# Kernel tuning notes

Measured on AMD Instinct MI355X. Metric: run time of the kernel, lower is better.

## Reference

```python
import jax, jax.numpy as jnp
import numpy as np

POINT_DIM, VOXEL_DIM, NUM_HEADS = 3, 256, 8
HEAD_DIM = VOXEL_DIM // NUM_HEADS


def _linear_params(key, fan_in, fan_out):
    kw, kb = jax.random.split(key)
    bound = 1.0 / np.sqrt(fan_in)
    W = jax.random.uniform(kw, (fan_out, fan_in), jnp.float32, -bound, bound)
    b = jax.random.uniform(kb, (fan_out,), jnp.float32, -bound, bound)
    return W, b


def setup_inputs() -> dict:
    key = jax.random.key(0)
    ks = jax.random.split(key, 7)
    points = jax.random.normal(ks[0], (2, 4096, POINT_DIM), jnp.float32)
    voxel_features = jax.random.normal(ks[1], (2, 2048, VOXEL_DIM), jnp.float32)
    Wp, bp = _linear_params(ks[2], POINT_DIM, VOXEL_DIM)
    Wq, bq = _linear_params(ks[3], VOXEL_DIM, VOXEL_DIM)
    Wk, bk = _linear_params(ks[4], VOXEL_DIM, VOXEL_DIM)
    Wv, bv = _linear_params(ks[5], VOXEL_DIM, VOXEL_DIM)
    Wf, bf = _linear_params(ks[6], VOXEL_DIM * 2, VOXEL_DIM)
    return {
        "points": points, "voxel_features": voxel_features,
        "Wp": Wp, "bp": bp, "Wq": Wq, "bq": bq,
        "Wk": Wk, "bk": bk, "Wv": Wv, "bv": bv,
        "Wf": Wf, "bf": bf,
    }


def reference(points, voxel_features, Wp, bp, Wq, bq, Wk, bk, Wv, bv, Wf, bf):
    B, N, _ = points.shape
    M = voxel_features.shape[1]
    # projections (torch Linear: x @ W.T + b)
    point_features = points @ Wp.T + bp                      # [B,N,D]
    q = (point_features @ Wq.T + bq).reshape(B, N, NUM_HEADS, HEAD_DIM)
    k = (voxel_features @ Wk.T + bk).reshape(B, M, NUM_HEADS, HEAD_DIM)
    v = (voxel_features @ Wv.T + bv).reshape(B, M, NUM_HEADS, HEAD_DIM)
    # attention scores [B,H,N,M]
    scale = 1.0 / np.sqrt(HEAD_DIM).astype(np.float32)
    attn = jnp.einsum('bnhd,bmhd->bhnm', q, k) * scale
    attn = jax.nn.softmax(attn, axis=-1)
    attended = jnp.einsum('bhnm,bmhd->bnhd', attn, v).reshape(B, N, VOXEL_DIM)
    fused = jnp.concatenate([point_features, attended], axis=-1) @ Wf.T + bf
    return fused
```

## Files before the change

kernel.cpp:

```cpp
#include <hip/hip_runtime.h>

#define B_ 2
#define N_ 4096
#define M_ 2048
#define D_ 256
#define H_ 8
#define DH_ 32
#define ROWS_ (B_*N_)
#define KVROWS_ (B_*M_)
#define PRE_ (0.17677669529663687f * 1.4426950408889634f)
#define CBASE_ 32.0f

typedef __attribute__((ext_vector_type(8))) short short8_t;
typedef __attribute__((ext_vector_type(4))) float float4_t;

#if defined(__has_builtin)
# if __has_builtin(__builtin_amdgcn_exp2f)
#  define EXP2F(x) __builtin_amdgcn_exp2f(x)
# else
#  define EXP2F(x) exp2f(x)
# endif
#else
# define EXP2F(x) exp2f(x)
#endif

__device__ __forceinline__ unsigned int rne_u(float f) {
    union { float f; unsigned int u; } c;
    c.f = f;
    return c.u + 0x7FFFu + ((c.u >> 16) & 1u);
}

__device__ __forceinline__ unsigned short f2us(float f) {
    return (unsigned short)(rne_u(f) >> 16);
}

__device__ __forceinline__ unsigned int pack2rn(float a, float b) {
    return __builtin_amdgcn_perm(rne_u(b), rne_u(a), 0x07060302u);
}

__device__ __forceinline__ unsigned int pack2tr(float a, float b) {
    union { float f; unsigned int u; } x, y;
    x.f = a; y.f = b;
    return __builtin_amdgcn_perm(y.u, x.u, 0x07060302u);
}

__device__ __forceinline__ short8_t cvt8(float4 a, float4 b) {
    union { unsigned int u[4]; short8_t s; } c;
    c.u[0] = pack2rn(a.x, a.y);
    c.u[1] = pack2rn(a.z, a.w);
    c.u[2] = pack2rn(b.x, b.y);
    c.u[3] = pack2rn(b.z, b.w);
    return c.s;
}

__device__ __forceinline__ int xcd_swz(int bid, int nwg) {
    const int cpx = nwg >> 3;
    return (bid & 7) * cpx + (bid >> 3);
}

template<int K, int NCOL, int LDSRC>
__device__ __forceinline__ void stageB2(const float* __restrict__ W, int col0, int kof,
                                        unsigned short* __restrict__ Bs, int tid)
{
    const int n = tid & (NCOL - 1), g = tid / NCOL;
    const int GROUPS = 256 / NCOL;
    const int CPT = (K / 8) / GROUPS;
    const float* src = W + (size_t)(col0 + n) * LDSRC + kof + g * (K / GROUPS);
#pragma unroll
    for (int ci = 0; ci < CPT; ci++) {
        int logc = g * CPT + ci;
        int phys = logc ^ (n & 7);
        short8_t v = cvt8(*(const float4*)(src + ci * 8), *(const float4*)(src + ci * 8 + 4));
        *(short8_t*)(Bs + (size_t)n * K + phys * 8) = v;
    }
}

template<int K>
__device__ __forceinline__ short8_t readB(const unsigned short* __restrict__ Bs,
                                          int c, int l16, int quad, int k0)
{
    int phys = ((k0 >> 3) + quad) ^ (l16 & 7);
    return *(const short8_t*)(Bs + (size_t)(16 * c + l16) * K + phys * 8);
}

__global__ __launch_bounds__(256) void g_projkv4(
    const float* __restrict__ voxel,
    const float* __restrict__ Wp, const float* __restrict__ bp,
    const float* __restrict__ Wq, const float* __restrict__ bq,
    const float* __restrict__ Wk, const float* __restrict__ bk,
    const float* __restrict__ Wv, const float* __restrict__ bv,
    const float* __restrict__ Wf, const float* __restrict__ bfb,
    unsigned short* __restrict__ k_g, unsigned short* __restrict__ vt_g,
    float* __restrict__ Wqc, float* __restrict__ Wfc)
{
    const int tid = threadIdx.x;
    const int wave = tid >> 6, lane = tid & 63, quad = lane >> 4, l16 = lane & 15;

    __shared__ unsigned short Bs[64 * 256];

    const int bid = (int)blockIdx.x;
    if (bid < 512) {
        const int lbid = xcd_swz(bid, 512);
        const int row0 = (lbid >> 3) * 64;
        const int sub  = lbid & 7;
        const int col0 = (sub >> 1) * 64;
        const bool isV = sub & 1;

        stageB2<256, 64, 256>(isV ? Wv : Wk, col0, 0, Bs, tid);

        const float* arow = voxel + (size_t)(row0 + wave * 16 + l16) * D_;
        short8_t af[8];
#pragma unroll
        for (int i = 0; i < 8; i++)
            af[i] = cvt8(*(const float4*)(arow + i * 32 + quad * 8),
                         *(const float4*)(arow + i * 32 + quad * 8 + 4));

        float4_t acc[4];
#pragma unroll
        for (int c = 0; c < 4; c++) acc[c] = (float4_t){0.f, 0.f, 0.f, 0.f};
        __syncthreads();
#pragma unroll
        for (int i = 0; i < 8; i++)
#pragma unroll
            for (int c = 0; c < 4; c++)
                acc[c] = __builtin_amdgcn_mfma_f32_16x16x32_bf16(af[i], readB<256>(Bs, c, l16, quad, i * 32), acc[c], 0, 0, 0);

        if (!isV) {
#pragma unroll
            for (int c = 0; c < 4; c++) {
                int col = col0 + 16 * c + l16;
                float bbk = bk[col];
#pragma unroll
                for (int r = 0; r < 4; r++) {
                    int row = row0 + wave * 16 + quad * 4 + r;
                    k_g[(size_t)row * D_ + col] = f2us(acc[c][r] + bbk);
                }
            }
        } else {
            const int b = row0 / M_;
            const int m0 = row0 - b * M_ + wave * 16 + quad * 4;
#pragma unroll
            for (int c = 0; c < 4; c++) {
                int col = col0 + 16 * c + l16;
                float bbv = bv[col];
                int h = col >> 5, dh = col & 31;
                unsigned int u0 = pack2rn(acc[c][0] + bbv, acc[c][1] + bbv);
                unsigned int u1 = pack2rn(acc[c][2] + bbv, acc[c][3] + bbv);
                *(uint2*)(vt_g + (size_t)((b * H_ + h) * DH_ + dh) * M_ + m0) = make_uint2(u0, u1);
            }
        }
    } else {
        const int role = bid - 512;
        float* wps = (float*)Bs;
        *(float4*)(wps + tid * 4) = make_float4(Wp[tid * 3 + 0], Wp[tid * 3 + 1],
                                                Wp[tid * 3 + 2], bp[tid]);
        __syncthreads();
        const int col = tid;
        const float* wrow = role ? (Wf + (size_t)col * 512) : (Wq + (size_t)col * 256);
        float a0 = 0.f, a1 = 0.f, a2 = 0.f, ab = 0.f;
#pragma unroll 4
        for (int d = 0; d < 256; d += 4) {
            float4 wv = *(const float4*)(wrow + d);
            float4 w0 = *(const float4*)(wps + (d + 0) * 4);
            float4 w1 = *(const float4*)(wps + (d + 1) * 4);
            float4 w2 = *(const float4*)(wps + (d + 2) * 4);
            float4 w3 = *(const float4*)(wps + (d + 3) * 4);
            a0 += wv.x * w0.x + wv.y * w1.x + wv.z * w2.x + wv.w * w3.x;
            a1 += wv.x * w0.y + wv.y * w1.y + wv.z * w2.y + wv.w * w3.y;
            a2 += wv.x * w0.z + wv.y * w1.z + wv.z * w2.z + wv.w * w3.z;
            ab += wv.x * w0.w + wv.y * w1.w + wv.z * w2.w + wv.w * w3.w;
        }
        if (role == 0) {
            *(float4*)(Wqc + (size_t)col * 4) =
                make_float4(a0 * PRE_, a1 * PRE_, a2 * PRE_, (ab + bq[col]) * PRE_);
        } else {
            *(float4*)(Wfc + (size_t)col * 4) =
                make_float4(a0, a1, a2, ab + bfb[col]);
        }
    }
}

__global__ __launch_bounds__(512) void k_attn11(
    const float* __restrict__ points, const float* __restrict__ Wqc,
    const unsigned short* __restrict__ k_g,
    const unsigned short* __restrict__ vt_g,
    unsigned short* __restrict__ att_g)
{
    const int tid = threadIdx.x;
    const int w = tid >> 6, lane = tid & 63, quad = lane >> 4, l16 = lane & 15;
    const int lbid = xcd_swz((int)blockIdx.x, B_ * H_ * (N_ / 128));
    const int nt = lbid & 31;
    const int bh = lbid >> 5;
    const int b = bh >> 3, h = bh & 7;
    const int n0 = nt * 128 + w * 16;

    __shared__ unsigned short Kt[4][64][40];
    __shared__ unsigned short Vt[4][32][72];

    const unsigned short* kbase = k_g + (size_t)(b * M_) * D_ + h * DH_;
    const unsigned short* vbase = vt_g + (size_t)(bh * DH_) * M_;

    const bool isK = (tid < 256);
    const int kr = tid >> 2, kc = tid & 3;
    const int vr = (tid - 256) >> 3, vc = tid & 7;
    const int ksr = kr ^ ((kr & 8) >> 1);

    const int gstep = isK ? 64 * D_ : 64;
    const unsigned short* gq = isK ? (kbase + (size_t)kr * D_ + kc * 8)
                                   : (vbase + (size_t)vr * M_ + vc * 8);
    unsigned short* ldst = isK ? (&Kt[0][0][0] + ksr * 40 + kc * 8)
                               : (&Vt[0][0][0] + vr * 72 + vc * 8);
    const int lstride = isK ? 2560 : 2304;

    *(short8_t*)ldst = *(const short8_t*)gq;
    gq += gstep;
    *(short8_t*)(ldst + lstride) = *(const short8_t*)gq;

    const int rbas = 8 * (l16 >> 2) + (l16 & 3);
    const int rx = l16 & 4;
    int krow[4];
#pragma unroll
    for (int t = 0; t < 4; t++)
        krow[t] = (rbas + 4 * (t & 1) + 32 * (t >> 1)) ^ rx;

    const size_t qrow = (size_t)(b * N_ + n0 + l16);
    const float p0 = points[qrow * 3 + 0];
    const float p1 = points[qrow * 3 + 1];
    const float p2 = points[qrow * 3 + 2];
    float q8[8];
#pragma unroll
    for (int j = 0; j < 8; j++) {
        float4 wc = *(const float4*)(Wqc + (size_t)(h * DH_ + quad * 8 + j) * 4);
        q8[j] = p0 * wc.x + p1 * wc.y + p2 * wc.z + wc.w;
    }
    short8_t qf = cvt8(make_float4(q8[0], q8[1], q8[2], q8[3]),
                       make_float4(q8[4], q8[5], q8[6], q8[7]));

    short8_t ones;
#pragma unroll
    for (int j = 0; j < 8; j++) ones[j] = (short)0x3F80;

    float4_t od0 = {0.f, 0.f, 0.f, 0.f};
    float4_t od1 = {0.f, 0.f, 0.f, 0.f};
    float4_t lacc = {0.f, 0.f, 0.f, 0.f};

    const float4_t zc = {-CBASE_, -CBASE_, -CBASE_, -CBASE_};

    __syncthreads();

#define STEPC(KB_, VB_)                                                         \
    do {                                                                        \
        float4_t st[4];                                                         \
        _Pragma("unroll")                                                       \
        for (int t = 0; t < 4; t++) {                                           \
            short8_t kf = *(const short8_t*)&Kt[KB_][krow[t]][quad * 8];        \
            st[t] = __builtin_amdgcn_mfma_f32_16x16x32_bf16(kf, qf, zc, 0, 0, 0); \
        }                                                                       \
        unsigned int uu[4][2];                                                  \
        _Pragma("unroll")                                                       \
        for (int t = 0; t < 4; t++) {                                           \
            float e0 = EXP2F(st[t][0]);                                         \
            float e1 = EXP2F(st[t][1]);                                         \
            float e2 = EXP2F(st[t][2]);                                         \
            float e3 = EXP2F(st[t][3]);                                         \
            uu[t][0] = pack2tr(e0, e1);                                         \
            uu[t][1] = pack2tr(e2, e3);                                         \
        }                                                                       \
        union { unsigned int u[4]; short8_t s; } pa, pb2;                       \
        pa.u[0]  = uu[0][0]; pa.u[1]  = uu[0][1];                               \
        pa.u[2]  = uu[1][0]; pa.u[3]  = uu[1][1];                               \
        pb2.u[0] = uu[2][0]; pb2.u[1] = uu[2][1];                               \
        pb2.u[2] = uu[3][0]; pb2.u[3] = uu[3][1];                               \
        lacc = __builtin_amdgcn_mfma_f32_16x16x32_bf16(ones, pa.s,  lacc, 0, 0, 0); \
        lacc = __builtin_amdgcn_mfma_f32_16x16x32_bf16(ones, pb2.s, lacc, 0, 0, 0); \
        short8_t vf00 = *(const short8_t*)&Vt[VB_][l16][quad * 8];              \
        short8_t vf01 = *(const short8_t*)&Vt[VB_][l16][32 + quad * 8];         \
        short8_t vf10 = *(const short8_t*)&Vt[VB_][16 + l16][quad * 8];         \
        short8_t vf11 = *(const short8_t*)&Vt[VB_][16 + l16][32 + quad * 8];    \
        od0 = __builtin_amdgcn_mfma_f32_16x16x32_bf16(vf00, pa.s,  od0, 0, 0, 0); \
        od0 = __builtin_amdgcn_mfma_f32_16x16x32_bf16(vf01, pb2.s, od0, 0, 0, 0); \
        od1 = __builtin_amdgcn_mfma_f32_16x16x32_bf16(vf10, pa.s,  od1, 0, 0, 0); \
        od1 = __builtin_amdgcn_mfma_f32_16x16x32_bf16(vf11, pb2.s, od1, 0, 0, 0); \
    } while (0)

#pragma unroll 2
    for (int s = 0; s < M_ / 64; s += 2) {
        const bool m0 = (s + 2 < M_ / 64);
        const bool m1 = (s + 3 < M_ / 64);
        short8_t nxt0, nxt1;
        if (m0) { gq += gstep; nxt0 = *(const short8_t*)gq; }
        if (m1) { gq += gstep; nxt1 = *(const short8_t*)gq; }

        STEPC((s) & 3, (s) & 3);
        STEPC((s + 1) & 3, (s + 1) & 3);

        if (m0) *(short8_t*)(ldst + ((s + 2) & 3) * lstride) = nxt0;
        if (m1) *(short8_t*)(ldst + ((s + 3) & 3) * lstride) = nxt1;
        __syncthreads();
    }
#undef STEPC

    const float inv = 1.0f / lacc[0];

    unsigned short* ob = att_g + (size_t)(b * N_ + n0 + l16) * D_ + h * DH_;
    {
        unsigned int u0 = pack2rn(od0[0] * inv, od0[1] * inv);
        unsigned int u1 = pack2rn(od0[2] * inv, od0[3] * inv);
        *(uint2*)(ob + quad * 4) = make_uint2(u0, u1);
        unsigned int u2 = pack2rn(od1[0] * inv, od1[1] * inv);
        unsigned int u3 = pack2rn(od1[2] * inv, od1[3] * inv);
        *(uint2*)(ob + 16 + quad * 4) = make_uint2(u2, u3);
    }
}

__global__ __launch_bounds__(256) void g_fuse3(
    const unsigned short* __restrict__ att_g,
    const float* __restrict__ points, const float* __restrict__ Wfc,
    const float* __restrict__ Wf,
    float* __restrict__ out)
{
    const int tid = threadIdx.x;
    const int wave = tid >> 6, lane = tid & 63, quad = lane >> 4, l16 = lane & 15;
    const int lbid = xcd_swz((int)blockIdx.x, (ROWS_ / 64) * 4);
    const int row0 = (lbid >> 2) * 64;
    const int col0 = (lbid & 3) * 64;

    __shared__ unsigned short Bs[64 * 256];

    stageB2<256, 64, 512>(Wf, col0, 256, Bs, tid);
    __syncthreads();

    float4_t acc[4];
#pragma unroll
    for (int c = 0; c < 4; c++) acc[c] = (float4_t){0.f, 0.f, 0.f, 0.f};

    const size_t arow = (size_t)(row0 + wave * 16 + l16) * D_;
#pragma unroll
    for (int k0 = 0; k0 < 256; k0 += 32) {
        short8_t af = *(const short8_t*)(att_g + arow + k0 + quad * 8);
#pragma unroll
        for (int c = 0; c < 4; c++)
            acc[c] = __builtin_amdgcn_mfma_f32_16x16x32_bf16(af, readB<256>(Bs, c, l16, quad, k0), acc[c], 0, 0, 0);
    }

    const int rbase = row0 + wave * 16 + quad * 4;
    float px[4], py[4], pz[4];
#pragma unroll
    for (int r = 0; r < 4; r++) {
        px[r] = points[(size_t)(rbase + r) * 3 + 0];
        py[r] = points[(size_t)(rbase + r) * 3 + 1];
        pz[r] = points[(size_t)(rbase + r) * 3 + 2];
    }
#pragma unroll
    for (int c = 0; c < 4; c++) {
        int col = col0 + 16 * c + l16;
        float4 wf = *(const float4*)(Wfc + (size_t)col * 4);
#pragma unroll
        for (int r = 0; r < 4; r++) {
            out[(size_t)(rbase + r) * D_ + col] =
                acc[c][r] + px[r] * wf.x + py[r] * wf.y + pz[r] * wf.z + wf.w;
        }
    }
}

extern "C" void kernel_launch(void* const* d_in, const int* in_sizes, int n_in,
                              void* d_out, int out_size, void* d_ws, size_t ws_size,
                              hipStream_t stream)
{
    const float* points = (const float*)d_in[0];
    const float* voxel  = (const float*)d_in[1];
    const float* Wp  = (const float*)d_in[2];
    const float* bp  = (const float*)d_in[3];
    const float* Wq  = (const float*)d_in[4];
    const float* bq  = (const float*)d_in[5];
    const float* Wk  = (const float*)d_in[6];
    const float* bk  = (const float*)d_in[7];
    const float* Wv  = (const float*)d_in[8];
    const float* bv  = (const float*)d_in[9];
    const float* Wf  = (const float*)d_in[10];
    const float* bfb = (const float*)d_in[11];
    float* out = (float*)d_out;

    float* Wqc = (float*)d_ws;
    float* Wfc = Wqc + 256 * 4;
    unsigned short* k_g   = (unsigned short*)(Wfc + 256 * 4);
    unsigned short* vt_g  = k_g  + (size_t)KVROWS_ * D_;
    unsigned short* att_g = vt_g + (size_t)KVROWS_ * D_;

    g_projkv4<<<dim3(514), dim3(256), 0, stream>>>(voxel, Wp, bp, Wq, bq, Wk, bk,
                                                   Wv, bv, Wf, bfb, k_g, vt_g, Wqc, Wfc);
    k_attn11<<<dim3(B_ * H_ * (N_ / 128)), dim3(512), 0, stream>>>(points, Wqc, k_g, vt_g, att_g);
    g_fuse3 <<<dim3((ROWS_ / 64) * 4), dim3(256), 0, stream>>>(att_g, points, Wfc, Wf, out);
}
```

Before: 132.1 us.

## Fold query projection into keys to cut attention score dot to rank four

Since each query is an affine function of three point coordinates, q·k equals [p,1]·(Wqc^T k). The projection kernel now computes a per-head four-element vector per key, Wqc^T k, instead of storing full K rows. The attention kernel then loads this compact kq tile for the whole sequence into LDS once and computes scores with a masked MFMA. This removes the K stream and its double-buffered staging from the attention loop and leaves only V streaming, so LDS per block shrinks and launch bounds are raised for occupancy. In exchange, the projection epilogue gains a shuffle reduction and a serial Wqc prologue. Scores are also computed from bf16-rounded products, which may change numerical accuracy.

```diff
diff --git a/kernel.cpp b/kernel.cpp
--- a/kernel.cpp
+++ b/kernel.cpp
@@ -83,20 +83,21 @@
     return *(const short8_t*)(Bs + (size_t)(16 * c + l16) * K + phys * 8);
 }
 
-__global__ __launch_bounds__(256) void g_projkv4(
+__global__ __launch_bounds__(256) void g_projkv5(
     const float* __restrict__ voxel,
     const float* __restrict__ Wp, const float* __restrict__ bp,
     const float* __restrict__ Wq, const float* __restrict__ bq,
     const float* __restrict__ Wk, const float* __restrict__ bk,
     const float* __restrict__ Wv, const float* __restrict__ bv,
     const float* __restrict__ Wf, const float* __restrict__ bfb,
-    unsigned short* __restrict__ k_g, unsigned short* __restrict__ vt_g,
-    float* __restrict__ Wqc, float* __restrict__ Wfc)
+    unsigned short* __restrict__ kq_g, unsigned short* __restrict__ vt_g,
+    float* __restrict__ Wfc)
 {
     const int tid = threadIdx.x;
     const int wave = tid >> 6, lane = tid & 63, quad = lane >> 4, l16 = lane & 15;
 
     __shared__ unsigned short Bs[64 * 256];
+    __shared__ float Wqc_l[64 * 4];
 
     const int bid = (int)blockIdx.x;
     if (bid < 512) {
@@ -106,6 +107,42 @@
         const int col0 = (sub >> 1) * 64;
         const bool isV = sub & 1;
 
+        if (!isV) {
+            float* wps = (float*)Bs;
+            float* P4  = (float*)Bs + 1024;
+            *(float4*)(wps + tid * 4) = make_float4(Wp[tid * 3 + 0], Wp[tid * 3 + 1],
+                                                    Wp[tid * 3 + 2], bp[tid]);
+            __syncthreads();
+            {
+                const int cc = tid >> 2, part = tid & 3;
+                const float* wrow = Wq + (size_t)(col0 + cc) * 256 + part * 64;
+                const float* wpp = wps + part * 256;
+                float a0 = 0.f, a1 = 0.f, a2 = 0.f, ab = 0.f;
+#pragma unroll 4
+                for (int e = 0; e < 64; e++) {
+                    float wv = wrow[e];
+                    float4 aa = *(const float4*)(wpp + e * 4);
+                    a0 += wv * aa.x; a1 += wv * aa.y; a2 += wv * aa.z; ab += wv * aa.w;
+                }
+                *(float4*)(P4 + (size_t)tid * 4) = make_float4(a0, a1, a2, ab);
+            }
+            __syncthreads();
+            if (tid < 64) {
+                float4 s0 = *(const float4*)(P4 + (tid * 4 + 0) * 4);
+                float4 s1 = *(const float4*)(P4 + (tid * 4 + 1) * 4);
+                float4 s2 = *(const float4*)(P4 + (tid * 4 + 2) * 4);
+                float4 s3 = *(const float4*)(P4 + (tid * 4 + 3) * 4);
+                float a0 = (s0.x + s1.x) + (s2.x + s3.x);
+                float a1 = (s0.y + s1.y) + (s2.y + s3.y);
+                float a2 = (s0.z + s1.z) + (s2.z + s3.z);
+                float ab = (s0.w + s1.w) + (s2.w + s3.w);
+                *(float4*)(Wqc_l + tid * 4) =
+                    make_float4(a0 * PRE_, a1 * PRE_, a2 * PRE_,
+                                (ab + bq[col0 + tid]) * PRE_);
+            }
+            __syncthreads();
+        }
+
         stageB2<256, 64, 256>(isV ? Wv : Wk, col0, 0, Bs, tid);
 
         const float* arow = voxel + (size_t)(row0 + wave * 16 + l16) * D_;
@@ -125,18 +162,7 @@
             for (int c = 0; c < 4; c++)
                 acc[c] = __builtin_amdgcn_mfma_f32_16x16x32_bf16(af[i], readB<256>(Bs, c, l16, quad, i * 32), acc[c], 0, 0, 0);
 
-        if (!isV) {
-#pragma unroll
-            for (int c = 0; c < 4; c++) {
-                int col = col0 + 16 * c + l16;
-                float bbk = bk[col];
-#pragma unroll
-                for (int r = 0; r < 4; r++) {
-                    int row = row0 + wave * 16 + quad * 4 + r;
-                    k_g[(size_t)row * D_ + col] = f2us(acc[c][r] + bbk);
-                }
-            }
-        } else {
+        if (isV) {
             const int b = row0 / M_;
             const int m0 = row0 - b * M_ + wave * 16 + quad * 4;
 #pragma unroll
@@ -148,15 +174,60 @@
                 unsigned int u1 = pack2rn(acc[c][2] + bbv, acc[c][3] + bbv);
                 *(uint2*)(vt_g + (size_t)((b * H_ + h) * DH_ + dh) * M_ + m0) = make_uint2(u0, u1);
             }
+        } else {
+            float bkv[4];
+#pragma unroll
+            for (int c = 0; c < 4; c++) bkv[c] = bk[col0 + 16 * c + l16];
+            float4 wq0 = *(const float4*)(Wqc_l + l16 * 4);
+            float4 wq1 = *(const float4*)(Wqc_l + (16 + l16) * 4);
+            float4 wq2 = *(const float4*)(Wqc_l + (32 + l16) * 4);
+            float4 wq3 = *(const float4*)(Wqc_l + (48 + l16) * 4);
+            const float* q0 = (const float*)&wq0;
+            const float* q1 = (const float*)&wq1;
+            const float* q2 = (const float*)&wq2;
+            const float* q3 = (const float*)&wq3;
+            float pA[4][4], pB[4][4];
+#pragma unroll
+            for (int r = 0; r < 4; r++) {
+                float kA0 = acc[0][r] + bkv[0], kA1 = acc[1][r] + bkv[1];
+                float kB0 = acc[2][r] + bkv[2], kB1 = acc[3][r] + bkv[3];
+#pragma unroll
+                for (int j = 0; j < 4; j++) {
+                    pA[r][j] = kA0 * q0[j] + kA1 * q1[j];
+                    pB[r][j] = kB0 * q2[j] + kB1 * q3[j];
+                }
+            }
+#pragma unroll
+            for (int m = 1; m < 16; m <<= 1)
+#pragma unroll
+                for (int r = 0; r < 4; r++)
+#pragma unroll
+                    for (int j = 0; j < 4; j++) {
+                        pA[r][j] += __shfl_xor(pA[r][j], m);
+                        pB[r][j] += __shfl_xor(pB[r][j], m);
+                    }
+            if (l16 == 0) {
+                const int b = row0 >> 11;
+                const int m0 = (row0 & (M_ - 1)) + wave * 16 + quad * 4;
+                const int hA = col0 >> 5;
+#pragma unroll
+                for (int r = 0; r < 4; r++) {
+                    unsigned int u0 = pack2rn(pA[r][0], pA[r][1]);
+                    unsigned int u1 = pack2rn(pA[r][2], pA[r][3]);
+                    *(uint2*)(kq_g + ((size_t)(b * H_ + hA) * M_ + m0 + r) * 4) = make_uint2(u0, u1);
+                    unsigned int u2 = pack2rn(pB[r][0], pB[r][1]);
+                    unsigned int u3 = pack2rn(pB[r][2], pB[r][3]);
+                    *(uint2*)(kq_g + ((size_t)(b * H_ + hA + 1) * M_ + m0 + r) * 4) = make_uint2(u2, u3);
+                }
+            }
         }
     } else {
-        const int role = bid - 512;
         float* wps = (float*)Bs;
         *(float4*)(wps + tid * 4) = make_float4(Wp[tid * 3 + 0], Wp[tid * 3 + 1],
                                                 Wp[tid * 3 + 2], bp[tid]);
         __syncthreads();
         const int col = tid;
-        const float* wrow = role ? (Wf + (size_t)col * 512) : (Wq + (size_t)col * 256);
+        const float* wrow = Wf + (size_t)col * 512;
         float a0 = 0.f, a1 = 0.f, a2 = 0.f, ab = 0.f;
 #pragma unroll 4
         for (int d = 0; d < 256; d += 4) {
@@ -170,91 +241,77 @@
             a2 += wv.x * w0.z + wv.y * w1.z + wv.z * w2.z + wv.w * w3.z;
             ab += wv.x * w0.w + wv.y * w1.w + wv.z * w2.w + wv.w * w3.w;
         }
-        if (role == 0) {
-            *(float4*)(Wqc + (size_t)col * 4) =
-                make_float4(a0 * PRE_, a1 * PRE_, a2 * PRE_, (ab + bq[col]) * PRE_);
-        } else {
-            *(float4*)(Wfc + (size_t)col * 4) =
-                make_float4(a0, a1, a2, ab + bfb[col]);
-        }
-    }
-}
-
-__global__ __launch_bounds__(512) void k_attn11(
-    const float* __restrict__ points, const float* __restrict__ Wqc,
-    const unsigned short* __restrict__ k_g,
+        *(float4*)(Wfc + (size_t)col * 4) = make_float4(a0, a1, a2, ab + bfb[col]);
+    }
+}
+
+__global__ __launch_bounds__(512, 8) void k_attn12(
+    const float* __restrict__ points,
+    const unsigned short* __restrict__ kq_g,
     const unsigned short* __restrict__ vt_g,
     unsigned short* __restrict__ att_g)
 {
     const int tid = threadIdx.x;
     const int w = tid >> 6, lane = tid & 63, quad = lane >> 4, l16 = lane & 15;
-    const int lbid = xcd_swz((int)blockIdx.x, B_ * H_ * (N_ / 128));
+    const int lbid = xcd_swz((int)blockIdx.x, 512);
     const int nt = lbid & 31;
     const int bh = lbid >> 5;
-    const int b = bh >> 3, h = bh & 7;
+    const int b = bh >> 3;
     const int n0 = nt * 128 + w * 16;
 
-    __shared__ unsigned short Kt[4][64][40];
-    __shared__ unsigned short Vt[4][32][72];
-
-    const unsigned short* kbase = k_g + (size_t)(b * M_) * D_ + h * DH_;
-    const unsigned short* vbase = vt_g + (size_t)(bh * DH_) * M_;
-
-    const bool isK = (tid < 256);
-    const int kr = tid >> 2, kc = tid & 3;
-    const int vr = (tid - 256) >> 3, vc = tid & 7;
-    const int ksr = kr ^ ((kr & 8) >> 1);
-
-    const int gstep = isK ? 64 * D_ : 64;
-    const unsigned short* gq = isK ? (kbase + (size_t)kr * D_ + kc * 8)
-                                   : (vbase + (size_t)vr * M_ + vc * 8);
-    unsigned short* ldst = isK ? (&Kt[0][0][0] + ksr * 40 + kc * 8)
-                               : (&Vt[0][0][0] + vr * 72 + vc * 8);
-    const int lstride = isK ? 2560 : 2304;
-
-    *(short8_t*)ldst = *(const short8_t*)gq;
-    gq += gstep;
-    *(short8_t*)(ldst + lstride) = *(const short8_t*)gq;
-
-    const int rbas = 8 * (l16 >> 2) + (l16 & 3);
-    const int rx = l16 & 4;
-    int krow[4];
-#pragma unroll
-    for (int t = 0; t < 4; t++)
-        krow[t] = (rbas + 4 * (t & 1) + 32 * (t >> 1)) ^ rx;
+    __shared__ unsigned short SL[17408];
+    unsigned short* kqL = SL;
+    unsigned short* Vt  = SL + 8192;
+
+    {
+        const unsigned short* ksrc = kq_g + (size_t)bh * (M_ * 4);
+        const int off = tid * 16;
+        *(short8_t*)(kqL + off)     = *(const short8_t*)(ksrc + off);
+        *(short8_t*)(kqL + off + 8) = *(const short8_t*)(ksrc + off + 8);
+    }
+
+    const unsigned short* vbase = vt_g + (size_t)bh * DH_ * M_;
+    const int vr = (tid & 255) >> 3, vc = tid & 7;
+    const int half = tid >> 8;
+    unsigned short* vdst = Vt + vr * 72 + vc * 8;
+    const unsigned short* gqv = vbase + (size_t)vr * M_ + vc * 8;
+    *(short8_t*)(vdst + half * 2304) = *(const short8_t*)(gqv + half * 64);
+    gqv += (2 + half) * 64;
 
     const size_t qrow = (size_t)(b * N_ + n0 + l16);
     const float p0 = points[qrow * 3 + 0];
     const float p1 = points[qrow * 3 + 1];
     const float p2 = points[qrow * 3 + 2];
-    float q8[8];
-#pragma unroll
-    for (int j = 0; j < 8; j++) {
-        float4 wc = *(const float4*)(Wqc + (size_t)(h * DH_ + quad * 8 + j) * 4);
-        q8[j] = p0 * wc.x + p1 * wc.y + p2 * wc.z + wc.w;
-    }
-    short8_t qf = cvt8(make_float4(q8[0], q8[1], q8[2], q8[3]),
-                       make_float4(q8[4], q8[5], q8[6], q8[7]));
+    const unsigned int um = (quad == 0) ? 0xFFFFFFFFu : 0u;
+    union { unsigned int u[4]; short8_t s; } qfu;
+    qfu.u[0] = pack2rn(p0, p1) & um;
+    qfu.u[1] = pack2rn(p2, 1.0f) & um;
+    qfu.u[2] = 0u; qfu.u[3] = 0u;
+    const short8_t qf = qfu.s;
 
     short8_t ones;
 #pragma unroll
     for (int j = 0; j < 8; j++) ones[j] = (short)0x3F80;
+
+    const unsigned short* kqp = kqL + (8 * (l16 >> 2) + (l16 & 3)) * 4;
 
     float4_t od0 = {0.f, 0.f, 0.f, 0.f};
     float4_t od1 = {0.f, 0.f, 0.f, 0.f};
     float4_t lacc = {0.f, 0.f, 0.f, 0.f};
-
     const float4_t zc = {-CBASE_, -CBASE_, -CBASE_, -CBASE_};
 
     __syncthreads();
 
-#define STEPC(KB_, VB_)                                                         \
+#define STEPC(VB_, KQP_)                                                        \
     do {                                                                        \
         float4_t st[4];                                                         \
         _Pragma("unroll")                                                       \
         for (int t = 0; t < 4; t++) {                                           \
-            short8_t kf = *(const short8_t*)&Kt[KB_][krow[t]][quad * 8];        \
-            st[t] = __builtin_amdgcn_mfma_f32_16x16x32_bf16(kf, qf, zc, 0, 0, 0); \
+            uint2 kv2 = *(const uint2*)((KQP_) + (t & 1) * 16 + (t >> 1) * 128);\
+            union { unsigned int u[4]; short8_t s; } afu;                       \
+            afu.u[0] = kv2.x & um; afu.u[1] = kv2.y & um;                       \
+            afu.u[2] = 0u; afu.u[3] = 0u;                                       \
+            st[t] = __builtin_amdgcn_mfma_f32_16x16x32_bf16(afu.s, qf, zc, 0, 0, 0); \
         }                                                                       \
         unsigned int uu[4][2];                                                  \
         _Pragma("unroll")                                                       \
@@ -267,16 +324,14 @@
             uu[t][1] = pack2tr(e2, e3);                                         \
         }                                                                       \
         union { unsigned int u[4]; short8_t s; } pa, pb2;                       \
-        pa.u[0]  = uu[0][0]; pa.u[1]  = uu[0][1];                               \
-        pa.u[2]  = uu[1][0]; pa.u[3]  = uu[1][1];                               \
-        pb2.u[0] = uu[2][0]; pb2.u[1] = uu[2][1];                               \
-        pb2.u[2] = uu[3][0]; pb2.u[3] = uu[3][1];                               \
+        pa.u[0]  = uu[0][0]; pa.u[1]  = uu[0][1]; pa.u[2]  = uu[1][0]; pa.u[3]  = uu[1][1]; \
+        pb2.u[0] = uu[2][0]; pb2.u[1] = uu[2][1]; pb2.u[2] = uu[3][0]; pb2.u[3] = uu[3][1]; \
         lacc = __builtin_amdgcn_mfma_f32_16x16x32_bf16(ones, pa.s,  lacc, 0, 0, 0); \
         lacc = __builtin_amdgcn_mfma_f32_16x16x32_bf16(ones, pb2.s, lacc, 0, 0, 0); \
-        short8_t vf00 = *(const short8_t*)&Vt[VB_][l16][quad * 8];              \
-        short8_t vf01 = *(const short8_t*)&Vt[VB_][l16][32 + quad * 8];         \
-        short8_t vf10 = *(const short8_t*)&Vt[VB_][16 + l16][quad * 8];         \
-        short8_t vf11 = *(const short8_t*)&Vt[VB_][16 + l16][32 + quad * 8];    \
+        short8_t vf00 = *(const short8_t*)(Vt + (VB_) * 2304 + l16 * 72 + quad * 8);        \
+        short8_t vf01 = *(const short8_t*)(Vt + (VB_) * 2304 + l16 * 72 + 32 + quad * 8);   \
+        short8_t vf10 = *(const short8_t*)(Vt + (VB_) * 2304 + (16 + l16) * 72 + quad * 8); \
+        short8_t vf11 = *(const short8_t*)(Vt + (VB_) * 2304 + (16 + l16) * 72 + 32 + quad * 8); \
         od0 = __builtin_amdgcn_mfma_f32_16x16x32_bf16(vf00, pa.s,  od0, 0, 0, 0); \
         od0 = __builtin_amdgcn_mfma_f32_16x16x32_bf16(vf01, pb2.s, od0, 0, 0, 0); \
         od1 = __builtin_amdgcn_mfma_f32_16x16x32_bf16(vf10, pa.s,  od1, 0, 0, 0); \
@@ -285,24 +340,25 @@
 
 #pragma unroll 2
     for (int s = 0; s < M_ / 64; s += 2) {
-        const bool m0 = (s + 2 < M_ / 64);
-        const bool m1 = (s + 3 < M_ / 64);
-        short8_t nxt0, nxt1;
-        if (m0) { gq += gstep; nxt0 = *(const short8_t*)gq; }
-        if (m1) { gq += gstep; nxt1 = *(const short8_t*)gq; }
-
-        STEPC((s) & 3, (s) & 3);
-        STEPC((s + 1) & 3, (s + 1) & 3);
-
-        if (m0) *(short8_t*)(ldst + ((s + 2) & 3) * lstride) = nxt0;
-        if (m1) *(short8_t*)(ldst + ((s + 3) & 3) * lstride) = nxt1;
+        const int tgt = s + 2 + half;
+        short8_t nxt;
+        if (tgt < M_ / 64) nxt = *(const short8_t*)gqv;
+
+        STEPC((s) & 3, kqp);
+        STEPC((s + 1) & 3, (kqp + 256));
+
+        if (tgt < M_ / 64) {
+            *(short8_t*)(vdst + (tgt & 3) * 2304) = nxt;
+            gqv += 128;
+        }
+        kqp += 512;
         __syncthreads();
     }
 #undef STEPC
 
     const float inv = 1.0f / lacc[0];
 
-    unsigned short* ob = att_g + (size_t)(b * N_ + n0 + l16) * D_ + h * DH_;
+    unsigned short* ob = att_g + (size_t)(b * N_ + n0 + l16) * D_ + (bh & 7) * DH_;
     {
         unsigned int u0 = pack2rn(od0[0] * inv, od0[1] * inv);
         unsigned int u1 = pack2rn(od0[2] * inv, od0[3] * inv);
@@ -381,14 +437,13 @@
     const float* bfb = (const float*)d_in[11];
     float* out = (float*)d_out;
 
-    float* Wqc = (float*)d_ws;
-    float* Wfc = Wqc + 256 * 4;
-    unsigned short* k_g   = (unsigned short*)(Wfc + 256 * 4);
-    unsigned short* vt_g  = k_g  + (size_t)KVROWS_ * D_;
+    float* Wfc = (float*)d_ws;
+    unsigned short* kq_g  = (unsigned short*)(Wfc + 256 * 4);
+    unsigned short* vt_g  = kq_g + (size_t)B_ * H_ * M_ * 4;
     unsigned short* att_g = vt_g + (size_t)KVROWS_ * D_;
 
-    g_projkv4<<<dim3(514), dim3(256), 0, stream>>>(voxel, Wp, bp, Wq, bq, Wk, bk,
-                                                   Wv, bv, Wf, bfb, k_g, vt_g, Wqc, Wfc);
-    k_attn11<<<dim3(B_ * H_ * (N_ / 128)), dim3(512), 0, stream>>>(points, Wqc, k_g, vt_g, att_g);
+    g_projkv5<<<dim3(513), dim3(256), 0, stream>>>(voxel, Wp, bp, Wq, bq, Wk, bk,
+                                                   Wv, bv, Wf, bfb, kq_g, vt_g, Wfc);
+    k_attn12<<<dim3(512), dim3(512), 0, stream>>>(points, kq_g, vt_g, att_g);
     g_fuse3 <<<dim3((ROWS_ / 64) * 4), dim3(256), 0, stream>>>(att_g, points, Wfc, Wf, out);
 }
```

After: 145.5 us. 1.1x slower.

## Split attention KV range in two and merge partial outputs in fuse kernel

Applied to the files above, without the earlier changes.

The attention kernel now splits the key/value sequence into two halves, doubling the grid so each block processes half of M. Each half writes unnormalized fp32 partial outputs and partial softmax denominators to workspace. The fusion kernel sums the two partials, normalizes, converts to bf16 and feeds the output GEMM. The aim is more parallelism and better CU fill, paid for with extra fp32 global memory traffic and a larger workspace; the merge is only correct because the softmax uses a fixed offset rather than a per-row running max.

```diff
diff --git a/kernel.cpp b/kernel.cpp
--- a/kernel.cpp
+++ b/kernel.cpp
@@ -8,6 +8,8 @@
 #define DH_ 32
 #define ROWS_ (B_*N_)
 #define KVROWS_ (B_*M_)
+#define ODHALF_ ((size_t)ROWS_*D_)
+#define LHALF_ ((size_t)B_*H_*N_)
 #define PRE_ (0.17677669529663687f * 1.4426950408889634f)
 #define CBASE_ 32.0f
 
@@ -180,25 +182,26 @@
     }
 }
 
-__global__ __launch_bounds__(512) void k_attn11(
+__global__ __launch_bounds__(512) void k_attn13(
     const float* __restrict__ points, const float* __restrict__ Wqc,
     const unsigned short* __restrict__ k_g,
     const unsigned short* __restrict__ vt_g,
-    unsigned short* __restrict__ att_g)
+    float* __restrict__ od_g, float* __restrict__ l_g)
 {
     const int tid = threadIdx.x;
     const int w = tid >> 6, lane = tid & 63, quad = lane >> 4, l16 = lane & 15;
-    const int lbid = xcd_swz((int)blockIdx.x, B_ * H_ * (N_ / 128));
-    const int nt = lbid & 31;
-    const int bh = lbid >> 5;
+    const int lbid = xcd_swz((int)blockIdx.x, B_ * H_ * (N_ / 128) * 2);
+    const int mh = lbid & 1;
+    const int nt = (lbid >> 1) & 31;
+    const int bh = lbid >> 6;
     const int b = bh >> 3, h = bh & 7;
     const int n0 = nt * 128 + w * 16;
 
     __shared__ unsigned short Kt[4][64][40];
     __shared__ unsigned short Vt[4][32][72];
 
-    const unsigned short* kbase = k_g + (size_t)(b * M_) * D_ + h * DH_;
-    const unsigned short* vbase = vt_g + (size_t)(bh * DH_) * M_;
+    const unsigned short* kbase = k_g + ((size_t)b * M_ + mh * (M_ / 2)) * D_ + h * DH_;
+    const unsigned short* vbase = vt_g + (size_t)bh * DH_ * M_ + mh * (M_ / 2);
 
     const bool isK = (tid < 256);
     const int kr = tid >> 2, kc = tid & 3;
@@ -284,9 +287,9 @@
     } while (0)
 
 #pragma unroll 2
-    for (int s = 0; s < M_ / 64; s += 2) {
-        const bool m0 = (s + 2 < M_ / 64);
-        const bool m1 = (s + 3 < M_ / 64);
+    for (int s = 0; s < M_ / 128; s += 2) {
+        const bool m0 = (s + 2 < M_ / 128);
+        const bool m1 = (s + 3 < M_ / 128);
         short8_t nxt0, nxt1;
         if (m0) { gq += gstep; nxt0 = *(const short8_t*)gq; }
         if (m1) { gq += gstep; nxt1 = *(const short8_t*)gq; }
@@ -300,21 +303,15 @@
     }
 #undef STEPC
 
-    const float inv = 1.0f / lacc[0];
-
-    unsigned short* ob = att_g + (size_t)(b * N_ + n0 + l16) * D_ + h * DH_;
-    {
-        unsigned int u0 = pack2rn(od0[0] * inv, od0[1] * inv);
-        unsigned int u1 = pack2rn(od0[2] * inv, od0[3] * inv);
-        *(uint2*)(ob + quad * 4) = make_uint2(u0, u1);
-        unsigned int u2 = pack2rn(od1[0] * inv, od1[1] * inv);
-        unsigned int u3 = pack2rn(od1[2] * inv, od1[3] * inv);
-        *(uint2*)(ob + 16 + quad * 4) = make_uint2(u2, u3);
-    }
-}
-
-__global__ __launch_bounds__(256) void g_fuse3(
-    const unsigned short* __restrict__ att_g,
+    float* obf = od_g + (size_t)mh * ODHALF_ + (size_t)(b * N_ + n0 + l16) * D_ + h * DH_;
+    *(float4_t*)(obf + quad * 4) = od0;
+    *(float4_t*)(obf + 16 + quad * 4) = od1;
+    if (quad == 0)
+        l_g[(size_t)mh * LHALF_ + (size_t)bh * N_ + n0 + l16] = lacc[0];
+}
+
+__global__ __launch_bounds__(256) void g_fuse4(
+    const float* __restrict__ od_g, const float* __restrict__ l_g,
     const float* __restrict__ points, const float* __restrict__ Wfc,
     const float* __restrict__ Wf,
     float* __restrict__ out)
@@ -328,16 +325,36 @@
     __shared__ unsigned short Bs[64 * 256];
 
     stageB2<256, 64, 512>(Wf, col0, 256, Bs, tid);
+
+    const int rowA = row0 + wave * 16 + l16;
+    const int bA = rowA >> 12, nA = rowA & (N_ - 1);
+    float inv[8];
+#pragma unroll
+    for (int hh = 0; hh < 8; hh++) {
+        size_t li = (size_t)(bA * H_ + hh) * N_ + nA;
+        inv[hh] = 1.0f / (l_g[li] + l_g[li + LHALF_]);
+    }
+
     __syncthreads();
 
     float4_t acc[4];
 #pragma unroll
     for (int c = 0; c < 4; c++) acc[c] = (float4_t){0.f, 0.f, 0.f, 0.f};
 
-    const size_t arow = (size_t)(row0 + wave * 16 + l16) * D_;
+    const size_t odrow = (size_t)rowA * D_;
 #pragma unroll
     for (int k0 = 0; k0 < 256; k0 += 32) {
-        short8_t af = *(const short8_t*)(att_g + arow + k0 + quad * 8);
+        const float iv = inv[k0 >> 5];
+        const float* pa = od_g + odrow + k0 + quad * 8;
+        float4 a0 = *(const float4*)(pa);
+        float4 a1 = *(const float4*)(pa + 4);
+        float4 c0 = *(const float4*)(pa + ODHALF_);
+        float4 c1 = *(const float4*)(pa + ODHALF_ + 4);
+        short8_t af = cvt8(
+            make_float4((a0.x + c0.x) * iv, (a0.y + c0.y) * iv,
+                        (a0.z + c0.z) * iv, (a0.w + c0.w) * iv),
+            make_float4((a1.x + c1.x) * iv, (a1.y + c1.y) * iv,
+                        (a1.z + c1.z) * iv, (a1.w + c1.w) * iv));
 #pragma unroll
         for (int c = 0; c < 4; c++)
             acc[c] = __builtin_amdgcn_mfma_f32_16x16x32_bf16(af, readB<256>(Bs, c, l16, quad, k0), acc[c], 0, 0, 0);
@@ -385,10 +402,11 @@
     float* Wfc = Wqc + 256 * 4;
     unsigned short* k_g   = (unsigned short*)(Wfc + 256 * 4);
     unsigned short* vt_g  = k_g  + (size_t)KVROWS_ * D_;
-    unsigned short* att_g = vt_g + (size_t)KVROWS_ * D_;
+    float* od_g = (float*)(vt_g + (size_t)KVROWS_ * D_);
+    float* l_g  = od_g + 2 * ODHALF_;
 
     g_projkv4<<<dim3(514), dim3(256), 0, stream>>>(voxel, Wp, bp, Wq, bq, Wk, bk,
                                                    Wv, bv, Wf, bfb, k_g, vt_g, Wqc, Wfc);
-    k_attn11<<<dim3(B_ * H_ * (N_ / 128)), dim3(512), 0, stream>>>(points, Wqc, k_g, vt_g, att_g);
-    g_fuse3 <<<dim3((ROWS_ / 64) * 4), dim3(256), 0, stream>>>(att_g, points, Wfc, Wf, out);
-}
+    k_attn13<<<dim3(B_ * H_ * (N_ / 128) * 2), dim3(512), 0, stream>>>(points, Wqc, k_g, vt_g, od_g, l_g);
+    g_fuse4 <<<dim3((ROWS_ / 64) * 4), dim3(256), 0, stream>>>(od_g, l_g, points, Wfc, Wf, out);
+}
```

After: 144.7 us. +9.5%, slower.

## Load K/V tiles directly from global into registers, dropping LDS staging

Applied to the files above, without the earlier changes.

The attention kernel no longer stages K and V tiles through shared memory with block-wide barriers. Each wave now loads its MFMA operand fragments straight from global memory into registers, using a two-deep register double buffer to overlap loads with compute. Block size is halved to 256 threads (64 query rows) with a doubled grid and a launch-bounds occupancy hint. This removes LDS traffic and __syncthreads, but each wave now fetches K/V independently, so global/L2 traffic rises about fourfold per query tile and the loads are less coalesced.

```diff
diff --git a/kernel.cpp b/kernel.cpp
--- a/kernel.cpp
+++ b/kernel.cpp
@@ -180,7 +180,7 @@
     }
 }
 
-__global__ __launch_bounds__(512) void k_attn11(
+__global__ __launch_bounds__(256, 4) void k_attn14(
     const float* __restrict__ points, const float* __restrict__ Wqc,
     const unsigned short* __restrict__ k_g,
     const unsigned short* __restrict__ vt_g,
@@ -188,40 +188,20 @@
 {
     const int tid = threadIdx.x;
     const int w = tid >> 6, lane = tid & 63, quad = lane >> 4, l16 = lane & 15;
-    const int lbid = xcd_swz((int)blockIdx.x, B_ * H_ * (N_ / 128));
-    const int nt = lbid & 31;
-    const int bh = lbid >> 5;
+    const int lbid = xcd_swz((int)blockIdx.x, B_ * H_ * (N_ / 64));
+    const int nt = lbid & 63;
+    const int bh = lbid >> 6;
     const int b = bh >> 3, h = bh & 7;
-    const int n0 = nt * 128 + w * 16;
-
-    __shared__ unsigned short Kt[4][64][40];
-    __shared__ unsigned short Vt[4][32][72];
+    const int n0 = nt * 64 + w * 16;
 
     const unsigned short* kbase = k_g + (size_t)(b * M_) * D_ + h * DH_;
-    const unsigned short* vbase = vt_g + (size_t)(bh * DH_) * M_;
-
-    const bool isK = (tid < 256);
-    const int kr = tid >> 2, kc = tid & 3;
-    const int vr = (tid - 256) >> 3, vc = tid & 7;
-    const int ksr = kr ^ ((kr & 8) >> 1);
-
-    const int gstep = isK ? 64 * D_ : 64;
-    const unsigned short* gq = isK ? (kbase + (size_t)kr * D_ + kc * 8)
-                                   : (vbase + (size_t)vr * M_ + vc * 8);
-    unsigned short* ldst = isK ? (&Kt[0][0][0] + ksr * 40 + kc * 8)
-                               : (&Vt[0][0][0] + vr * 72 + vc * 8);
-    const int lstride = isK ? 2560 : 2304;
-
-    *(short8_t*)ldst = *(const short8_t*)gq;
-    gq += gstep;
-    *(short8_t*)(ldst + lstride) = *(const short8_t*)gq;
-
-    const int rbas = 8 * (l16 >> 2) + (l16 & 3);
-    const int rx = l16 & 4;
-    int krow[4];
-#pragma unroll
-    for (int t = 0; t < 4; t++)
-        krow[t] = (rbas + 4 * (t & 1) + 32 * (t >> 1)) ^ rx;
+    const unsigned short* vbase = vt_g + (size_t)bh * DH_ * M_;
+
+    const int g0 = 8 * (l16 >> 2) + (l16 & 3);
+    const unsigned short* kp0 = kbase + (size_t)g0 * D_ + quad * 8;
+    const unsigned short* kp2 = kp0 + 32 * D_;
+    const unsigned short* vp0 = vbase + (size_t)l16 * M_ + quad * 8;
+    const unsigned short* vp1 = vp0 + (size_t)16 * M_;
 
     const size_t qrow = (size_t)(b * N_ + n0 + l16);
     const float p0 = points[qrow * 3 + 0];
@@ -243,19 +223,30 @@
     float4_t od0 = {0.f, 0.f, 0.f, 0.f};
     float4_t od1 = {0.f, 0.f, 0.f, 0.f};
     float4_t lacc = {0.f, 0.f, 0.f, 0.f};
-
     const float4_t zc = {-CBASE_, -CBASE_, -CBASE_, -CBASE_};
 
-    __syncthreads();
-
-#define STEPC(KB_, VB_)                                                         \
+    short8_t kA[4], vA[4], kB[4], vB[4];
+
+#define LOADS(KR, VR, S_)                                                    \
+    do {                                                                     \
+        const size_t ko = (size_t)(S_) * (64 * D_);                          \
+        const size_t vo = (size_t)(S_) * 64;                                 \
+        KR[0] = *(const short8_t*)(kp0 + ko);                                \
+        KR[1] = *(const short8_t*)(kp0 + ko + 4 * D_);                       \
+        KR[2] = *(const short8_t*)(kp2 + ko);                                \
+        KR[3] = *(const short8_t*)(kp2 + ko + 4 * D_);                       \
+        VR[0] = *(const short8_t*)(vp0 + vo);                                \
+        VR[1] = *(const short8_t*)(vp0 + vo + 32);                           \
+        VR[2] = *(const short8_t*)(vp1 + vo);                                \
+        VR[3] = *(const short8_t*)(vp1 + vo + 32);                           \
+    } while (0)
+
+#define COMPUTE(KR, VR)                                                         \
     do {                                                                        \
         float4_t st[4];                                                         \
         _Pragma("unroll")                                                       \
-        for (int t = 0; t < 4; t++) {                                           \
-            short8_t kf = *(const short8_t*)&Kt[KB_][krow[t]][quad * 8];        \
-            st[t] = __builtin_amdgcn_mfma_f32_16x16x32_bf16(kf, qf, zc, 0, 0, 0); \
-        }                                                                       \
+        for (int t = 0; t < 4; t++)                                             \
+            st[t] = __builtin_amdgcn_mfma_f32_16x16x32_bf16(KR[t], qf, zc, 0, 0, 0); \
         unsigned int uu[4][2];                                                  \
         _Pragma("unroll")                                                       \
         for (int t = 0; t < 4; t++) {                                           \
@@ -273,32 +264,21 @@
         pb2.u[2] = uu[3][0]; pb2.u[3] = uu[3][1];                               \
         lacc = __builtin_amdgcn_mfma_f32_16x16x32_bf16(ones, pa.s,  lacc, 0, 0, 0); \
         lacc = __builtin_amdgcn_mfma_f32_16x16x32_bf16(ones, pb2.s, lacc, 0, 0, 0); \
-        short8_t vf00 = *(const short8_t*)&Vt[VB_][l16][quad * 8];              \
-        short8_t vf01 = *(const short8_t*)&Vt[VB_][l16][32 + quad * 8];         \
-        short8_t vf10 = *(const short8_t*)&Vt[VB_][16 + l16][quad * 8];         \
-        short8_t vf11 = *(const short8_t*)&Vt[VB_][16 + l16][32 + quad * 8];    \
-        od0 = __builtin_amdgcn_mfma_f32_16x16x32_bf16(vf00, pa.s,  od0, 0, 0, 0); \
-        od0 = __builtin_amdgcn_mfma_f32_16x16x32_bf16(vf01, pb2.s, od0, 0, 0, 0); \
-        od1 = __builtin_amdgcn_mfma_f32_16x16x32_bf16(vf10, pa.s,  od1, 0, 0, 0); \
-        od1 = __builtin_amdgcn_mfma_f32_16x16x32_bf16(vf11, pb2.s, od1, 0, 0, 0); \
+        od0 = __builtin_amdgcn_mfma_f32_16x16x32_bf16(VR[0], pa.s,  od0, 0, 0, 0); \
+        od0 = __builtin_amdgcn_mfma_f32_16x16x32_bf16(VR[1], pb2.s, od0, 0, 0, 0); \
+        od1 = __builtin_amdgcn_mfma_f32_16x16x32_bf16(VR[2], pa.s,  od1, 0, 0, 0); \
+        od1 = __builtin_amdgcn_mfma_f32_16x16x32_bf16(VR[3], pb2.s, od1, 0, 0, 0); \
     } while (0)
 
-#pragma unroll 2
+    LOADS(kA, vA, 0);
     for (int s = 0; s < M_ / 64; s += 2) {
-        const bool m0 = (s + 2 < M_ / 64);
-        const bool m1 = (s + 3 < M_ / 64);
-        short8_t nxt0, nxt1;
-        if (m0) { gq += gstep; nxt0 = *(const short8_t*)gq; }
-        if (m1) { gq += gstep; nxt1 = *(const short8_t*)gq; }
-
-        STEPC((s) & 3, (s) & 3);
-        STEPC((s + 1) & 3, (s + 1) & 3);
-
-        if (m0) *(short8_t*)(ldst + ((s + 2) & 3) * lstride) = nxt0;
-        if (m1) *(short8_t*)(ldst + ((s + 3) & 3) * lstride) = nxt1;
-        __syncthreads();
-    }
-#undef STEPC
+        LOADS(kB, vB, s + 1);
+        COMPUTE(kA, vA);
+        if (s + 2 < M_ / 64) LOADS(kA, vA, s + 2);
+        COMPUTE(kB, vB);
+    }
+#undef LOADS
+#undef COMPUTE
 
     const float inv = 1.0f / lacc[0];
 
@@ -389,6 +369,6 @@
 
     g_projkv4<<<dim3(514), dim3(256), 0, stream>>>(voxel, Wp, bp, Wq, bq, Wk, bk,
                                                    Wv, bv, Wf, bfb, k_g, vt_g, Wqc, Wfc);
-    k_attn11<<<dim3(B_ * H_ * (N_ / 128)), dim3(512), 0, stream>>>(points, Wqc, k_g, vt_g, att_g);
+    k_attn14<<<dim3(B_ * H_ * (N_ / 64)), dim3(256), 0, stream>>>(points, Wqc, k_g, vt_g, att_g);
     g_fuse3 <<<dim3((ROWS_ / 64) * 4), dim3(256), 0, stream>>>(att_g, points, Wfc, Wf, out);
 }
```

Result: slower. 220.7 us (+67.0%).
